# Optimization experiments

Measured on AMD Instinct MI355X. Metric: run time of the kernel, lower is better.

## Reference

```python
import math
import jax, jax.numpy as jnp
import numpy as np

HIDDEN_DIM = 256
NEG_INF = -1e30


def setup_inputs() -> dict:
    key = jax.random.key(0)
    k1, k2, k3, k4 = jax.random.split(key, 4)
    B, L_IN, L_MEM, D_IN, D_MEM = 16, 2048, 2048, 512, 512
    inputs = jax.random.normal(k1, (B, L_IN, D_IN), dtype=jnp.float32)
    memory = jax.random.normal(k2, (B, L_MEM, D_MEM), dtype=jnp.float32)
    memory_mask = jnp.ones((B, L_MEM), dtype=jnp.int32)
    W_in = jax.random.normal(k3, (D_IN, HIDDEN_DIM), dtype=jnp.float32) * (1.0 / math.sqrt(D_IN))
    W_mem = jax.random.normal(k4, (D_MEM, HIDDEN_DIM), dtype=jnp.float32) * (1.0 / math.sqrt(D_MEM))
    return {"inputs": inputs, "memory": memory, "memory_mask": memory_mask,
            "W_in": W_in, "W_mem": W_mem}


def reference(inputs, memory, memory_mask, W_in, W_mem):
    # Projections: Linear(bias=False) + ReLU (dropout is identity at drop_prob=0)
    inp_h = jax.nn.relu(jnp.einsum('bld,dh->blh', inputs, W_in))    # [B, L_in, H]
    mem_h = jax.nn.relu(jnp.einsum('bmd,dh->bmh', memory, W_mem))   # [B, L_mem, H]
    # Scaled dot-product scores
    scale = 1.0 / math.sqrt(HIDDEN_DIM)
    logits = jnp.einsum('blh,bmh->blm', inp_h, mem_h) * scale        # [B, L_in, L_mem]
    # Masked softmax over memory axis (mask broadcast over query axis)
    mask = (memory_mask > 0)[:, None, :]                             # [B, 1, L_mem]
    logits = jnp.where(mask, logits, NEG_INF)
    score = jax.nn.softmax(logits, axis=-1)                          # [B, L_in, L_mem]
    # Context over the ORIGINAL (unprojected) memory, then concat with inputs
    context = jnp.einsum('blm,bmd->bld', score, memory)              # [B, L_in, D_mem]
    return jnp.concatenate([context, inputs], axis=-1)               # [B, L_in, D_mem+D_in]
```

## Files before the change

kernel.cpp:

```cpp
#include <hip/hip_runtime.h>
#include <cstdint>
#include <cstddef>

typedef _Float16 f16;
typedef __attribute__((ext_vector_type(4)))  _Float16 f16x4;
typedef __attribute__((ext_vector_type(8)))  _Float16 f16x8;
typedef __attribute__((ext_vector_type(2)))  __fp16   fp16v2;
typedef __attribute__((ext_vector_type(4)))  float    f32x4;
typedef __attribute__((ext_vector_type(16))) float    f32x16;

static constexpr int BB = 16, LL = 2048, DIN = 512, HH = 256, DOUT = 1024;
static constexpr float SCALE = 0.0625f;
#define MASKVAL (-30000.0f)

#define BAR()    __builtin_amdgcn_s_barrier()
#define SCHED0() __builtin_amdgcn_sched_barrier(0)

__device__ __forceinline__ void gload16(const void* g, void* l) {
  __builtin_amdgcn_global_load_lds(
      (const __attribute__((address_space(1))) unsigned int*)g,
      (__attribute__((address_space(3))) unsigned int*)l, 16, 0, 0);
}

__device__ __forceinline__ unsigned pk2(float a, float b) {
  union { fp16v2 v; unsigned u; } c;
  c.v = __builtin_amdgcn_cvt_pkrtz(a, b);
  return c.u;
}

__global__ void wt2_kernel(const float* __restrict__ Wa, const float* __restrict__ Wb,
                           f16* __restrict__ WTa, f16* __restrict__ WTb) {
  int g = blockIdx.x * 256 + threadIdx.x;
  const float* W = (g < 131072) ? Wa : Wb;
  f16* WT = (g < 131072) ? WTa : WTb;
  int gg = g & 131071;
  int d = gg >> 8, h = gg & 255;
  WT[h * 512 + d] = (f16)W[gg];
}

__global__ void vt_kernel(const float* __restrict__ mem, f16* __restrict__ VT) {
  int m0 = blockIdx.x * 32, d0 = blockIdx.y * 32, b = blockIdx.z;
  __shared__ f16 t[32][36];
  int tid = threadIdx.x;
  {
    int r = tid >> 3, c4 = (tid & 7) * 4;
    float4 v = *(const float4*)(mem + (size_t)(b * LL + m0 + r) * DIN + d0 + c4);
    t[c4 + 0][r] = (f16)v.x; t[c4 + 1][r] = (f16)v.y;
    t[c4 + 2][r] = (f16)v.z; t[c4 + 3][r] = (f16)v.w;
  }
  __syncthreads();
  {
    int d = tid >> 3, seg = tid & 7;
    f16x4 hv = *(const f16x4*)&t[d][seg * 4];
    *(f16x4*)(VT + (size_t)(b * 512 + d0 + d) * 2048 + m0 + seg * 4) = hv;
  }
}

__global__ __launch_bounds__(256, 2) void proj_kernel(const float* __restrict__ Xa,
                                                      const float* __restrict__ Xb,
                                                      const f16* __restrict__ WTa,
                                                      const f16* __restrict__ WTb,
                                                      f16* __restrict__ Oa,
                                                      f16* __restrict__ Ob) {
  const float* X = blockIdx.z ? Xb : Xa;
  const f16* WT  = blockIdx.z ? WTb : WTa;
  f16* Out       = blockIdx.z ? Ob : Oa;
  const int Rbase = blockIdx.x * 128, Cbase = blockIdx.y * 128;
  __shared__ f16 a_t[128 * 40];
  __shared__ f16 b_t[128 * 32];
  const int tid = threadIdx.x, lane = tid & 63, wave = tid >> 6;
  const int wr = wave >> 1, wc = wave & 1;
  const int l15 = lane & 15, g4 = lane >> 4;
  f32x4 acc[4][4] = {};
  for (int ks = 0; ks < 16; ++ks) {
    __syncthreads();
#pragma unroll
    for (int k = 0; k < 4; ++k) {
      int idx = k * 256 + tid;
      int row = idx >> 3, c4 = idx & 7;
      float4 v = *(const float4*)(X + (size_t)(Rbase + row) * 512 + ks * 32 + c4 * 4);
      f16x4 hv = { (f16)v.x, (f16)v.y, (f16)v.z, (f16)v.w };
      *(f16x4*)((char*)a_t + row * 80 + c4 * 8) = hv;
    }
#pragma unroll
    for (int i = 0; i < 2; ++i) {
      int o = i * 4096 + wave * 1024 + lane * 16;
      int r = o >> 6, cp = o & 63;
      gload16((const char*)WT + (size_t)(Cbase + r) * 1024 + ks * 64 + (cp ^ ((r & 3) << 4)),
              (char*)b_t + i * 4096 + wave * 1024);
    }
    __syncthreads();
    f16x8 af[4], bf[4];
#pragma unroll
    for (int mi = 0; mi < 4; ++mi) {
      int r = wr * 64 + mi * 16 + l15;
      af[mi] = *(const f16x8*)((const char*)a_t + r * 80 + g4 * 16);
    }
#pragma unroll
    for (int ni = 0; ni < 4; ++ni) {
      int r = wc * 64 + ni * 16 + l15;
      bf[ni] = *(const f16x8*)((const char*)b_t + r * 64 + ((g4 * 16) ^ ((r & 3) << 4)));
    }
#pragma unroll
    for (int mi = 0; mi < 4; ++mi)
#pragma unroll
      for (int ni = 0; ni < 4; ++ni)
        acc[mi][ni] = __builtin_amdgcn_mfma_f32_16x16x32_f16(af[mi], bf[ni], acc[mi][ni], 0, 0, 0);
  }
#pragma unroll
  for (int mi = 0; mi < 4; ++mi)
#pragma unroll
    for (int ni = 0; ni < 4; ++ni)
#pragma unroll
      for (int di = 0; di < 4; ++di) {
        int row = Rbase + wr * 64 + mi * 16 + g4 * 4 + di;
        int col = Cbase + wc * 64 + ni * 16 + l15;
        float v = acc[mi][ni][di];
        Out[(size_t)row * 256 + col] = (f16)(v > 0.f ? v : 0.f);
      }
}

__global__ __launch_bounds__(256, 3) void sqk_kernel(
    const int* __restrict__ mask, const f16* __restrict__ Qh, const f16* __restrict__ Kh,
    f16* __restrict__ Sfrag, float2* __restrict__ Pstats) {
  const int bid = blockIdx.x;
  const int lb = (bid & 7) * 128 + (bid >> 3);
  const int qgrp = lb & 15, g = lb >> 4;
  const int ms = g & 3, b = g >> 2;
  const int tid = threadIdx.x, lane = tid & 63, wave = tid >> 6;
  const int hi = lane >> 5, l31 = lane & 31;
  __shared__ f16 Kt[2][32 * 256];

  const int qg = qgrp * 128 + wave * 32 + l31;
  f16x8 Qf[16];
  {
    const f16x8* qrow = (const f16x8*)(Qh + ((size_t)b * LL + qg) * HH);
#pragma unroll
    for (int c = 0; c < 16; ++c) Qf[c] = qrow[2 * c + hi];
  }
  const int* mrow = mask + b * LL;

  auto stageK = [&](int bufi, int mt) {
#pragma unroll
    for (int i = 0; i < 4; ++i) {
      int o = i * 4096 + tid * 16;
      int r = o >> 9, cp = o & 511;
      gload16((const char*)Kh + (size_t)(b * LL + mt * 32 + r) * 512 + (cp ^ ((r & 31) << 4)),
              (char*)Kt[bufi] + o);
    }
  };

  const int mt0 = ms * 16;
  stageK(0, mt0);
  __syncthreads();

  for (int i = 0; i < 16; ++i) {
    const int mt = mt0 + i;
    const int mbase = mt * 32;
    if (i) {
      asm volatile("s_waitcnt vmcnt(3)" ::: "memory");
      SCHED0(); BAR(); SCHED0();
    }
    stageK((i & 1) ^ 1, mt0 + ((i + 1) & 15));

    const char* kb = (const char*)Kt[i & 1];
    f32x16 s0 = {}, s1 = {};
#pragma unroll
    for (int c = 0; c < 8; ++c) {
      f16x8 kf0 = *(const f16x8*)(kb + l31 * 512 + (((2 * c) * 32 + hi * 16) ^ (l31 << 4)));
      f16x8 kf1 = *(const f16x8*)(kb + l31 * 512 + (((2 * c + 1) * 32 + hi * 16) ^ (l31 << 4)));
      s0 = __builtin_amdgcn_mfma_f32_32x32x16_f16(kf0, Qf[2 * c], s0, 0, 0, 0);
      s1 = __builtin_amdgcn_mfma_f32_32x32x16_f16(kf1, Qf[2 * c + 1], s1, 0, 0, 0);
    }
    f32x16 s;
#pragma unroll
    for (int r = 0; r < 16; ++r) s[r] = s0[r] + s1[r];

    float tmax = MASKVAL;
#pragma unroll
    for (int c2 = 0; c2 < 4; ++c2) {
      int4 mk = *(const int4*)(mrow + mbase + c2 * 8 + hi * 4);
      float x;
      x = s[4*c2+0] * SCALE; s[4*c2+0] = mk.x ? x : MASKVAL;
      x = s[4*c2+1] * SCALE; s[4*c2+1] = mk.y ? x : MASKVAL;
      x = s[4*c2+2] * SCALE; s[4*c2+2] = mk.z ? x : MASKVAL;
      x = s[4*c2+3] * SCALE; s[4*c2+3] = mk.w ? x : MASKVAL;
      tmax = fmaxf(tmax, fmaxf(fmaxf(s[4*c2+0], s[4*c2+1]), fmaxf(s[4*c2+2], s[4*c2+3])));
    }
    tmax = fmaxf(tmax, __shfl_xor(tmax, 32, 64));
    float tsum = 0.f;
#pragma unroll
    for (int r = 0; r < 16; ++r) {
      float e = __expf(s[r] - tmax);
      s[r] = e;
      tsum += e;
    }
    tsum += __shfl_xor(tsum, 32, 64);

    f16x8 pf[2];
#pragma unroll
    for (int j = 0; j < 2; ++j) {
      unsigned a0 = pk2(s[8*j+0], s[8*j+1]);
      unsigned a1 = pk2(s[8*j+2], s[8*j+3]);
      unsigned b0 = pk2(s[8*j+4], s[8*j+5]);
      unsigned b1 = pk2(s[8*j+6], s[8*j+7]);
      asm volatile("v_permlane32_swap_b32 %0, %1" : "+v"(a0), "+v"(b0));
      asm volatile("v_permlane32_swap_b32 %0, %1" : "+v"(a1), "+v"(b1));
      union { f16x8 v; unsigned u[4]; } un;
      un.u[0] = a0; un.u[1] = a1; un.u[2] = b0; un.u[3] = b1;
      pf[j] = un.v;
    }
    const size_t mtg = (size_t)b * 64 + mt;
#pragma unroll
    for (int j = 0; j < 2; ++j)
      *(f16x8*)((char*)Sfrag + ((mtg * 2 + j) * 2048 + qg) * 32 + hi * 16) = pf[j];
    if (hi == 0) {
      float2 st; st.x = tmax; st.y = tsum;
      Pstats[mtg * 2048 + qg] = st;
    }
  }
}

__global__ void stats_copy_kernel(const float* __restrict__ X, const float2* __restrict__ Pstats,
                                  float* __restrict__ Mrow, float* __restrict__ Linv,
                                  float* __restrict__ out) {
  const int g = blockIdx.x, b = blockIdx.y;
  const int tid = threadIdx.x;
  const int row = g * 64 + (tid >> 2), sub = tid & 3;
  float bm[16], bs[16];
  float M = MASKVAL;
#pragma unroll
  for (int i = 0; i < 16; ++i) {
    float2 p = Pstats[((size_t)b * 64 + sub * 16 + i) * 2048 + row];
    bm[i] = p.x; bs[i] = p.y;
    M = fmaxf(M, p.x);
  }
  M = fmaxf(M, __shfl_xor(M, 1, 64));
  M = fmaxf(M, __shfl_xor(M, 2, 64));
  float L = 0.f;
#pragma unroll
  for (int i = 0; i < 16; ++i) L += bs[i] * __expf(bm[i] - M);
  L += __shfl_xor(L, 1, 64);
  L += __shfl_xor(L, 2, 64);
  if (sub == 0) {
    Mrow[(size_t)b * 2048 + row] = M;
    Linv[(size_t)b * 2048 + row] = 1.f / L;
  }
#pragma unroll
  for (int it = 0; it < 32; ++it) {
    int idx = it * 256 + tid;
    int r = idx >> 7, c4 = idx & 127;
    *(float4*)(out + ((size_t)b * 2048 + g * 64 + r) * 1024 + 512 + c4 * 4) =
        *(const float4*)(X + ((size_t)b * 2048 + g * 64 + r) * 512 + c4 * 4);
  }
}

__global__ __launch_bounds__(512, 4) void pv_kernel(
    const f16* __restrict__ Sfrag, const float2* __restrict__ Pstats,
    const float* __restrict__ Mrow, const float* __restrict__ Linv,
    const f16* __restrict__ VT, float* __restrict__ out) {
  const int bid = blockIdx.x;
  const int lb = (bid & 7) * 64 + (bid >> 3);
  const int b = lb >> 5;
  const int rest = lb & 31;
  const int qt = rest & 15, dt = rest >> 4;
  const int tid = threadIdx.x, lane = tid & 63, wave = tid >> 6;
  const int hi = lane >> 5, l31 = lane & 31;
  const int qs = wave & 3, dh = wave >> 2;
  const int dvBase = dt * 256;
  const int qg = qt * 128 + qs * 32 + l31;
  __shared__ f16 Vt[2][256 * 32];

  auto stage = [&](int bufi, int mt) {
#pragma unroll
    for (int i = 0; i < 2; ++i) {
      int o = i * 8192 + tid * 16;
      int dv = o >> 6, cp = o & 63;
      gload16((const char*)VT + (size_t)(b * 512 + dvBase + dv) * 4096 + mt * 64 + (cp ^ (((dv >> 1) & 3) << 4)),
              (char*)Vt[bufi] + o);
    }
  };

  const float Mq = Mrow[(size_t)b * 2048 + qg];
  f32x16 acc[4] = {};

  stage(0, 0);
  const size_t mtg0 = (size_t)b * 64;
  float2 ps_c = Pstats[mtg0 * 2048 + qg];
  f16x8 pf0_c = *(const f16x8*)((const char*)Sfrag + ((mtg0 * 2 + 0) * 2048 + qg) * 32 + hi * 16);
  f16x8 pf1_c = *(const f16x8*)((const char*)Sfrag + ((mtg0 * 2 + 1) * 2048 + qg) * 32 + hi * 16);
  __syncthreads();

  for (int mt = 0; mt < 64; ++mt) {
    if (mt) {
      asm volatile("s_waitcnt vmcnt(3)" ::: "memory");
      SCHED0(); BAR(); SCHED0();
    }
    const int nmt = (mt + 1) & 63;
    stage((mt + 1) & 1, nmt);
    const size_t mtgn = (size_t)b * 64 + nmt;
    float2 ps_n = Pstats[mtgn * 2048 + qg];
    f16x8 pf0_n = *(const f16x8*)((const char*)Sfrag + ((mtgn * 2 + 0) * 2048 + qg) * 32 + hi * 16);
    f16x8 pf1_n = *(const f16x8*)((const char*)Sfrag + ((mtgn * 2 + 1) * 2048 + qg) * 32 + hi * 16);

    float fact = __expf(ps_c.x - Mq);
    f16 fh = (f16)fact;
    f16x8 fv = { fh, fh, fh, fh, fh, fh, fh, fh };
    f16x8 pA0 = pf0_c * fv;
    f16x8 pA1 = pf1_c * fv;

    const char* vb = (const char*)Vt[mt & 1];
#pragma unroll
    for (int dsub = 0; dsub < 4; ++dsub) {
      int dvl = dh * 128 + dsub * 32 + l31;
      f16x8 vf0 = *(const f16x8*)(vb + dvl * 64 + ((hi * 16) ^ (((dvl >> 1) & 3) << 4)));
      f16x8 vf1 = *(const f16x8*)(vb + dvl * 64 + ((32 + hi * 16) ^ (((dvl >> 1) & 3) << 4)));
      acc[dsub] = __builtin_amdgcn_mfma_f32_32x32x16_f16(pA0, vf0, acc[dsub], 0, 0, 0);
      acc[dsub] = __builtin_amdgcn_mfma_f32_32x32x16_f16(pA1, vf1, acc[dsub], 0, 0, 0);
    }
    ps_c = ps_n; pf0_c = pf0_n; pf1_c = pf1_n;
  }

  float linv = Linv[(size_t)b * 2048 + qg];
  float lr[16];
#pragma unroll
  for (int r = 0; r < 16; ++r) lr[r] = __shfl(linv, (r & 3) + 8 * (r >> 2) + 4 * hi, 32);
#pragma unroll
  for (int dsub = 0; dsub < 4; ++dsub) {
    int dv = dvBase + dh * 128 + dsub * 32 + l31;
#pragma unroll
    for (int r = 0; r < 16; ++r) {
      int q = qt * 128 + qs * 32 + (r & 3) + 8 * (r >> 2) + 4 * hi;
      out[((size_t)b * 2048 + q) * 1024 + dv] = acc[dsub][r] * lr[r];
    }
  }
}

extern "C" void kernel_launch(void* const* d_in, const int* in_sizes, int n_in,
                              void* d_out, int out_size, void* d_ws, size_t ws_size,
                              hipStream_t stream) {
  const float* inputs = (const float*)d_in[0];
  const float* memory = (const float*)d_in[1];
  const int*   mmask  = (const int*)d_in[2];
  const float* W_in   = (const float*)d_in[3];
  const float* W_mem  = (const float*)d_in[4];
  float* out = (float*)d_out;

  char* ws = (char*)d_ws;
  f16*    Qh     = (f16*)ws;
  f16*    Kh     = (f16*)(ws + (16ull << 20));
  f16*    VT     = (f16*)(ws + (32ull << 20));
  f16*    WTi    = (f16*)(ws + (64ull << 20));
  f16*    WTm    = (f16*)(ws + (64ull << 20) + (1u << 18));
  f16*    Sfrag  = (f16*)(ws + (68ull << 20));
  float2* Pstats = (float2*)(ws + (196ull << 20));
  float*  MrowP  = (float*)(ws + (212ull << 20));
  float*  LinvP  = (float*)(ws + (213ull << 20));

  wt2_kernel<<<1024, 256, 0, stream>>>(W_in, W_mem, WTi, WTm);
  vt_kernel<<<dim3(64, 16, 16), 256, 0, stream>>>(memory, VT);
  proj_kernel<<<dim3(256, 2, 2), 256, 0, stream>>>(inputs, memory, WTi, WTm, Qh, Kh);
  sqk_kernel<<<1024, 256, 0, stream>>>(mmask, Qh, Kh, Sfrag, Pstats);
  stats_copy_kernel<<<dim3(32, 16), 256, 0, stream>>>(inputs, Pstats, MrowP, LinvP, out);
  pv_kernel<<<512, 512, 0, stream>>>(Sfrag, Pstats, MrowP, LinvP, VT, out);
}
```

Baseline: 279.3 us.

## Double PV loop step to two memory tiles per barrier and add MFMA priority hints

The PV kernel now stages two 32-wide memory tiles of V per pipeline stage, doubling LDS to two slots per buffer. This halves the number of block barriers and waitcnt points across the 64-tile loop and issues more global loads per stage. s_setprio(1) is raised around the MFMA blocks in both the score kernel and the PV kernel, so that waves doing matrix math get issue priority over waves loading. The larger LDS footprint (64 KB per block) may limit how many blocks fit per CU under launch_bounds(512,4).

```diff
diff --git a/kernel.cpp b/kernel.cpp
--- a/kernel.cpp
+++ b/kernel.cpp
@@ -165,6 +165,7 @@
 
     const char* kb = (const char*)Kt[i & 1];
     f32x16 s0 = {}, s1 = {};
+    __builtin_amdgcn_s_setprio(1);
 #pragma unroll
     for (int c = 0; c < 8; ++c) {
       f16x8 kf0 = *(const f16x8*)(kb + l31 * 512 + (((2 * c) * 32 + hi * 16) ^ (l31 << 4)));
@@ -172,6 +173,7 @@
       s0 = __builtin_amdgcn_mfma_f32_32x32x16_f16(kf0, Qf[2 * c], s0, 0, 0, 0);
       s1 = __builtin_amdgcn_mfma_f32_32x32x16_f16(kf1, Qf[2 * c + 1], s1, 0, 0, 0);
     }
+    __builtin_amdgcn_s_setprio(0);
     f32x16 s;
 #pragma unroll
     for (int r = 0; r < 16; ++r) s[r] = s0[r] + s1[r];
@@ -269,47 +271,28 @@
   const int qs = wave & 3, dh = wave >> 2;
   const int dvBase = dt * 256;
   const int qg = qt * 128 + qs * 32 + l31;
-  __shared__ f16 Vt[2][256 * 32];
-
-  auto stage = [&](int bufi, int mt) {
+  __shared__ f16 Vt[2][2][256 * 32];
+
+  auto stage = [&](int bufi, int slot, int mt) {
 #pragma unroll
     for (int i = 0; i < 2; ++i) {
       int o = i * 8192 + tid * 16;
       int dv = o >> 6, cp = o & 63;
       gload16((const char*)VT + (size_t)(b * 512 + dvBase + dv) * 4096 + mt * 64 + (cp ^ (((dv >> 1) & 3) << 4)),
-              (char*)Vt[bufi] + o);
+              (char*)Vt[bufi][slot] + o);
     }
   };
 
   const float Mq = Mrow[(size_t)b * 2048 + qg];
   f32x16 acc[4] = {};
 
-  stage(0, 0);
-  const size_t mtg0 = (size_t)b * 64;
-  float2 ps_c = Pstats[mtg0 * 2048 + qg];
-  f16x8 pf0_c = *(const f16x8*)((const char*)Sfrag + ((mtg0 * 2 + 0) * 2048 + qg) * 32 + hi * 16);
-  f16x8 pf1_c = *(const f16x8*)((const char*)Sfrag + ((mtg0 * 2 + 1) * 2048 + qg) * 32 + hi * 16);
-  __syncthreads();
-
-  for (int mt = 0; mt < 64; ++mt) {
-    if (mt) {
-      asm volatile("s_waitcnt vmcnt(3)" ::: "memory");
-      SCHED0(); BAR(); SCHED0();
-    }
-    const int nmt = (mt + 1) & 63;
-    stage((mt + 1) & 1, nmt);
-    const size_t mtgn = (size_t)b * 64 + nmt;
-    float2 ps_n = Pstats[mtgn * 2048 + qg];
-    f16x8 pf0_n = *(const f16x8*)((const char*)Sfrag + ((mtgn * 2 + 0) * 2048 + qg) * 32 + hi * 16);
-    f16x8 pf1_n = *(const f16x8*)((const char*)Sfrag + ((mtgn * 2 + 1) * 2048 + qg) * 32 + hi * 16);
-
-    float fact = __expf(ps_c.x - Mq);
+  auto compute = [&](float2 ps, f16x8 pf0, f16x8 pf1, const char* vb) {
+    float fact = __expf(ps.x - Mq);
     f16 fh = (f16)fact;
     f16x8 fv = { fh, fh, fh, fh, fh, fh, fh, fh };
-    f16x8 pA0 = pf0_c * fv;
-    f16x8 pA1 = pf1_c * fv;
-
-    const char* vb = (const char*)Vt[mt & 1];
+    f16x8 pA0 = pf0 * fv;
+    f16x8 pA1 = pf1 * fv;
+    __builtin_amdgcn_s_setprio(1);
 #pragma unroll
     for (int dsub = 0; dsub < 4; ++dsub) {
       int dvl = dh * 128 + dsub * 32 + l31;
@@ -318,7 +301,41 @@
       acc[dsub] = __builtin_amdgcn_mfma_f32_32x32x16_f16(pA0, vf0, acc[dsub], 0, 0, 0);
       acc[dsub] = __builtin_amdgcn_mfma_f32_32x32x16_f16(pA1, vf1, acc[dsub], 0, 0, 0);
     }
-    ps_c = ps_n; pf0_c = pf0_n; pf1_c = pf1_n;
+    __builtin_amdgcn_s_setprio(0);
+  };
+
+  stage(0, 0, 0);
+  stage(0, 1, 1);
+  const size_t gb = (size_t)b * 64;
+  float2 ps_c0 = Pstats[(gb + 0) * 2048 + qg];
+  f16x8 pf0_c0 = *(const f16x8*)((const char*)Sfrag + (((gb + 0) * 2 + 0) * 2048 + qg) * 32 + hi * 16);
+  f16x8 pf1_c0 = *(const f16x8*)((const char*)Sfrag + (((gb + 0) * 2 + 1) * 2048 + qg) * 32 + hi * 16);
+  float2 ps_c1 = Pstats[(gb + 1) * 2048 + qg];
+  f16x8 pf0_c1 = *(const f16x8*)((const char*)Sfrag + (((gb + 1) * 2 + 0) * 2048 + qg) * 32 + hi * 16);
+  f16x8 pf1_c1 = *(const f16x8*)((const char*)Sfrag + (((gb + 1) * 2 + 1) * 2048 + qg) * 32 + hi * 16);
+  __syncthreads();
+
+  for (int p = 0; p < 32; ++p) {
+    if (p) {
+      asm volatile("s_waitcnt vmcnt(6)" ::: "memory");
+      SCHED0(); BAR(); SCHED0();
+    }
+    const int n0 = (2 * p + 2) & 63, n1 = (2 * p + 3) & 63;
+    stage((p + 1) & 1, 0, n0);
+    stage((p + 1) & 1, 1, n1);
+    const size_t g0 = gb + n0, g1 = gb + n1;
+    float2 ps_n0 = Pstats[g0 * 2048 + qg];
+    f16x8 pf0_n0 = *(const f16x8*)((const char*)Sfrag + ((g0 * 2 + 0) * 2048 + qg) * 32 + hi * 16);
+    f16x8 pf1_n0 = *(const f16x8*)((const char*)Sfrag + ((g0 * 2 + 1) * 2048 + qg) * 32 + hi * 16);
+    float2 ps_n1 = Pstats[g1 * 2048 + qg];
+    f16x8 pf0_n1 = *(const f16x8*)((const char*)Sfrag + ((g1 * 2 + 0) * 2048 + qg) * 32 + hi * 16);
+    f16x8 pf1_n1 = *(const f16x8*)((const char*)Sfrag + ((g1 * 2 + 1) * 2048 + qg) * 32 + hi * 16);
+
+    compute(ps_c0, pf0_c0, pf1_c0, (const char*)Vt[p & 1][0]);
+    compute(ps_c1, pf0_c1, pf1_c1, (const char*)Vt[p & 1][1]);
+
+    ps_c0 = ps_n0; pf0_c0 = pf0_n0; pf1_c0 = pf1_n0;
+    ps_c1 = ps_n1; pf0_c1 = pf0_n1; pf1_c1 = pf1_n1;
   }
 
   float linv = Linv[(size_t)b * 2048 + qg];
```

Measured after the change: 285.5 us. 2.2% more time.
